# Kernel tuning notes

Measured on AMD Instinct MI355X. Metric: run time of the kernel, lower is better.

The kernel has to match this reference:

```python
import jax, jax.numpy as jnp
import numpy as np

N_NODES = 100000
N_EDGES = 1600000
D_IN = 64
HID = 64
N_GRAPHS = 256


def _glorot(key, shape):
    lim = float(np.sqrt(6.0 / (shape[0] + shape[1])))
    return jax.random.uniform(key, shape, jnp.float32, -lim, lim)


def setup_inputs() -> dict:
    key = jax.random.key(0)
    ks = jax.random.split(key, 12)
    x = jax.random.normal(ks[0], (N_NODES, D_IN), jnp.float32)
    edge_index = jax.random.randint(ks[1], (2, N_EDGES), 0, N_NODES, jnp.int64)
    batch = jnp.sort(jax.random.randint(ks[2], (N_NODES,), 0, N_GRAPHS, jnp.int64))
    params = {
        'Wrel1': _glorot(ks[3], (D_IN, HID)), 'brel1': jnp.zeros((HID,), jnp.float32), 'Wroot1': _glorot(ks[4], (D_IN, HID)),
        'Wrel2': _glorot(ks[5], (HID, HID)), 'brel2': jnp.zeros((HID,), jnp.float32), 'Wroot2': _glorot(ks[6], (HID, HID)),
        'Wrel3': _glorot(ks[7], (HID, HID)), 'brel3': jnp.zeros((HID,), jnp.float32), 'Wroot3': _glorot(ks[8], (HID, HID)),
        'Wlin': _glorot(ks[9], (HID, HID)), 'blin': jnp.zeros((HID,), jnp.float32),
    }
    return {'x': x, 'edge_index': edge_index, 'batch': batch, **params}


def _graph_conv(x, src, dst, Wrel, brel, Wroot):
    # PyG GraphConv: lin_rel(sum_{j in N(i)} x_j) + lin_root(x_i); bias on lin_rel only.
    aggr = jax.ops.segment_sum(x[src], dst, num_segments=N_NODES)  # [N, d] gather+scatter-add
    return aggr @ Wrel + brel + x @ Wroot


def reference(x, edge_index, batch, Wrel1, brel1, Wroot1, Wrel2, brel2, Wroot2,
              Wrel3, brel3, Wroot3, Wlin, blin):
    src, dst = edge_index[0], edge_index[1]
    h = jax.nn.relu(_graph_conv(x, src, dst, Wrel1, brel1, Wroot1))
    h = jax.nn.relu(_graph_conv(h, src, dst, Wrel2, brel2, Wroot2))
    h = _graph_conv(h, src, dst, Wrel3, brel3, Wroot3)
    # global_mean_pool over graphs
    sums = jax.ops.segment_sum(h, batch, num_segments=N_GRAPHS)          # [G, HID]
    counts = jax.ops.segment_sum(jnp.ones((N_NODES,), h.dtype), batch, num_segments=N_GRAPHS)
    pooled = sums / jnp.maximum(counts, 1.0)[:, None]
    # dropout is identity in eval mode
    return pooled @ Wlin + blin
```

## Files before the change

### kernel.cpp

```cpp
#include <hip/hip_runtime.h>
#include <hip/hip_bf16.h>

#define NN 100000
#define NE 1600000
#define DD 64
#define NG 256
#define SHIFT 8
#define NBK 391
#define BCAP 4608
#define NSB 256
#define CHUNK 6250

typedef __attribute__((ext_vector_type(8))) short bf16x8;
typedef __attribute__((ext_vector_type(4))) float f32x4;
typedef __attribute__((ext_vector_type(8))) unsigned short ushort8v;

__device__ __forceinline__ float b2f(ushort u){
  unsigned v = ((unsigned)u) << 16;
  return __uint_as_float(v);
}
__device__ __forceinline__ ushort f2b(float f){
  __hip_bfloat16 b = __float2bfloat16(f);
  return *(ushort*)&b;
}

__global__ void k_wpack3(const float* __restrict__ Wr1, const float* __restrict__ Wo1,
                         const float* __restrict__ Wr2, const float* __restrict__ Wo2,
                         const float* __restrict__ Wr3, const float* __restrict__ Wo3,
                         ushort* __restrict__ wp, int* __restrict__ gcur){
  int i = blockIdx.x*256 + threadIdx.x;
  if (i < NBK) gcur[i] = i*BCAP;
  if (i >= 3*8192) return;
  int lay = i >> 13;
  int r = i & 8191;
  int j = r & 7, l = (r>>3) & 63, t = (r>>9) & 7, s = r >> 12;
  int k = s*32 + ((l>>4)<<3) + j;
  int col = t*16 + (l&15);
  const float* Wrel  = (lay==0) ? Wr1 : (lay==1) ? Wr2 : Wr3;
  const float* Wroot = (lay==0) ? Wo1 : (lay==1) ? Wo2 : Wo3;
  float v = (col < 64) ? Wrel[k*64 + col] : Wroot[k*64 + (col-64)];
  wp[i] = f2b(v);
}

__global__ __launch_bounds__(512) void k_bscatter(const int* __restrict__ src, const int* __restrict__ dst,
                           int* __restrict__ gcur, unsigned* __restrict__ ebuf){
  __shared__ int h[NBK];
  __shared__ int base[NBK];
  __shared__ int lcur[NBK];
  for (int i=threadIdx.x; i<NBK; i+=512) h[i]=0;
  __syncthreads();
  const int e0 = blockIdx.x*CHUNK;
  const int e1 = min(e0+CHUNK, NE);
  for (int e=e0+threadIdx.x; e<e1; e+=512) atomicAdd(&h[dst[e]>>SHIFT], 1);
  __syncthreads();
  for (int i=threadIdx.x; i<NBK; i+=512){
    base[i] = h[i] ? atomicAdd(&gcur[i], h[i]) : 0;
    lcur[i] = 0;
  }
  __syncthreads();
  for (int e=e0+threadIdx.x; e<e1; e+=512){
    int d = dst[e];
    int b = d >> SHIFT;
    int r = atomicAdd(&lcur[b], 1);
    size_t idx = (size_t)base[b] + r;
    if (idx < (size_t)NBK*BCAP)
      ebuf[idx] = ((unsigned)(d & 255) << 17) | (unsigned)src[e];
  }
}

__global__ __launch_bounds__(512) void k_bfill(const unsigned* __restrict__ ebuf, const int* __restrict__ gcur,
                        int* __restrict__ rowptr, int* __restrict__ degarr, int* __restrict__ csr){
  __shared__ int c[256];
  __shared__ int lcur[256];
  __shared__ int s[256];
  __shared__ int scnt;
  const int b = blockIdx.x, t = threadIdx.x;
  const int ebase = b*BCAP;
  if (t == 0) scnt = min(gcur[b] - ebase, BCAP);
  if (t < 256) c[t] = 0;
  __syncthreads();
  const int cnt = scnt;
  for (int i=t; i<cnt; i+=512) atomicAdd(&c[ebuf[ebase+i]>>17], 1);
  __syncthreads();
  int v = (t < 256) ? c[t] : 0;
  if (t < 256) s[t] = v;
  __syncthreads();
  for (int off=1; off<256; off<<=1){
    int u = (t >= off && t < 256) ? s[t-off] : 0;
    __syncthreads();
    if (t < 256) s[t] += u;
    __syncthreads();
  }
  if (t < 256){
    int excl = s[t] - v;
    lcur[t] = excl;
    int node = (b << SHIFT) + t;
    if (node < NN){ rowptr[node] = ebase + excl; degarr[node] = v; }
  }
  __syncthreads();
  for (int i=t; i<cnt; i+=512){
    unsigned p = ebuf[ebase+i];
    int dl = (int)(p >> 17);
    int r = atomicAdd(&lcur[dl], 1);
    csr[ebase + r] = (int)(p & 0x1FFFFu);
  }
}

#define CPAD 136
__global__ __launch_bounds__(256) void k_gemm_mfma(const void* __restrict__ Av, int aIsF32,
    const ushort* __restrict__ wp, ushort* __restrict__ Y, ushort* __restrict__ Rr){
  __shared__ ushort ct[64*CPAD];
  const int tid = threadIdx.x;
  const int w = tid >> 6, l = tid & 63;
  const int m = l & 15, kg = l >> 4;
  const int row0 = blockIdx.x*64;
  int arow = row0 + w*16 + m; if (arow >= NN) arow = NN-1;
  bf16x8 a0, a1;
  if (aIsF32){
    const float* Af = (const float*)Av;
    float4 f0 = *(const float4*)&Af[(size_t)arow*64 + kg*8];
    float4 f1 = *(const float4*)&Af[(size_t)arow*64 + kg*8 + 4];
    float4 f2 = *(const float4*)&Af[(size_t)arow*64 + 32 + kg*8];
    float4 f3 = *(const float4*)&Af[(size_t)arow*64 + 32 + kg*8 + 4];
    a0[0]=(short)f2b(f0.x); a0[1]=(short)f2b(f0.y); a0[2]=(short)f2b(f0.z); a0[3]=(short)f2b(f0.w);
    a0[4]=(short)f2b(f1.x); a0[5]=(short)f2b(f1.y); a0[6]=(short)f2b(f1.z); a0[7]=(short)f2b(f1.w);
    a1[0]=(short)f2b(f2.x); a1[1]=(short)f2b(f2.y); a1[2]=(short)f2b(f2.z); a1[3]=(short)f2b(f2.w);
    a1[4]=(short)f2b(f3.x); a1[5]=(short)f2b(f3.y); a1[6]=(short)f2b(f3.z); a1[7]=(short)f2b(f3.w);
  } else {
    const ushort* Ab = (const ushort*)Av;
    a0 = *(const bf16x8*)&Ab[(size_t)arow*64 + kg*8];
    a1 = *(const bf16x8*)&Ab[(size_t)arow*64 + 32 + kg*8];
  }
  #pragma unroll
  for (int t=0; t<8; t++){
    bf16x8 b0 = *(const bf16x8*)&wp[((size_t)(0*8+t)*64 + l)*8];
    bf16x8 b1 = *(const bf16x8*)&wp[((size_t)(1*8+t)*64 + l)*8];
    f32x4 c = {0.f, 0.f, 0.f, 0.f};
    c = __builtin_amdgcn_mfma_f32_16x16x32_bf16(a0, b0, c, 0, 0, 0);
    c = __builtin_amdgcn_mfma_f32_16x16x32_bf16(a1, b1, c, 0, 0, 0);
    #pragma unroll
    for (int reg=0; reg<4; reg++){
      int lrow = w*16 + kg*4 + reg;
      ct[lrow*CPAD + t*16 + m] = f2b(c[reg]);
    }
  }
  __syncthreads();
  #pragma unroll
  for (int u=0; u<4; u++){
    int i = tid + u*256;
    int lrow = i >> 4, cb = i & 15;
    int grow = row0 + lrow;
    if (grow < NN){
      ushort8v v = *(const ushort8v*)&ct[lrow*CPAD + cb*8];
      if (cb < 8) *(ushort8v*)&Y [(size_t)grow*64 + cb*8]       = v;
      else        *(ushort8v*)&Rr[(size_t)grow*64 + (cb-8)*8]   = v;
    }
  }
}

__global__ __launch_bounds__(256) void k_aggr(const ushort* __restrict__ Y,
    const ushort* __restrict__ R, const float* __restrict__ brel,
    const int* __restrict__ rowptr, const int* __restrict__ degarr, const int* __restrict__ csr,
    ushort* __restrict__ hout, int do_relu){
  int node = blockIdx.x*4 + (threadIdx.x>>6);
  if (node >= NN) return;
  int lane = threadIdx.x & 63;
  int g = lane >> 3;
  int c8 = (lane & 7) << 3;
  int beg = rowptr[node];
  int dc = degarr[node];
  const int* lst = csr + beg;
  float a[8] = {0.f,0.f,0.f,0.f,0.f,0.f,0.f,0.f};
  int i = g;
  for (; i + 8 < dc; i += 16){
    int s0 = lst[i], s1 = lst[i+8];
    ushort8v y0 = *(const ushort8v*)&Y[((size_t)s0<<6) + c8];
    ushort8v y1 = *(const ushort8v*)&Y[((size_t)s1<<6) + c8];
    #pragma unroll
    for (int j=0;j<8;j++) a[j] += b2f(y0[j]) + b2f(y1[j]);
  }
  if (i < dc){
    int s0 = lst[i];
    ushort8v y0 = *(const ushort8v*)&Y[((size_t)s0<<6) + c8];
    #pragma unroll
    for (int j=0;j<8;j++) a[j] += b2f(y0[j]);
  }
  #pragma unroll
  for (int j=0;j<8;j++){
    a[j] += __shfl_xor(a[j], 8);
    a[j] += __shfl_xor(a[j], 16);
    a[j] += __shfl_xor(a[j], 32);
  }
  if (g == 0){
    ushort8v r8 = *(const ushort8v*)&R[((size_t)node<<6) + c8];
    float4 b0 = *(const float4*)&brel[c8];
    float4 b1 = *(const float4*)&brel[c8+4];
    float bb[8] = {b0.x,b0.y,b0.z,b0.w,b1.x,b1.y,b1.z,b1.w};
    ushort8v o;
    #pragma unroll
    for (int j=0;j<8;j++){
      float v = a[j] + b2f(r8[j]) + bb[j];
      if (do_relu) v = fmaxf(v, 0.f);
      o[j] = f2b(v);
    }
    *(ushort8v*)&hout[((size_t)node<<6) + c8] = o;
  }
}

__global__ __launch_bounds__(256) void k_pool(const ushort* __restrict__ h, const int* __restrict__ batch,
                       const float* __restrict__ Wlin, const float* __restrict__ blin,
                       float* __restrict__ out){
  int g = blockIdx.x;
  int lo=0, hi=NN;
  while (lo<hi){ int mid=(lo+hi)>>1; if (batch[mid] < g) lo=mid+1; else hi=mid; }
  int beg = lo;
  lo=0; hi=NN;
  while (lo<hi){ int mid=(lo+hi)>>1; if (batch[mid] < g+1) lo=mid+1; else hi=mid; }
  int end = lo;
  int lane = threadIdx.x & 63;
  int w = threadIdx.x >> 6;
  float acc = 0.f;
  for (int n = beg + w; n < end; n += 4) acc += b2f(h[(size_t)n*64 + lane]);
  __shared__ float red[4][64];
  __shared__ float p[64];
  red[w][lane] = acc;
  __syncthreads();
  if (w == 0){
    float v = red[0][lane]+red[1][lane]+red[2][lane]+red[3][lane];
    int cnt = end - beg;
    p[lane] = v / fmaxf((float)cnt, 1.f);
  }
  __syncthreads();
  if (w == 0){
    float o = blin[lane];
    #pragma unroll 8
    for (int k=0;k<64;k++) o += p[k]*Wlin[k*64+lane];
    out[g*64+lane] = o;
  }
}

extern "C" void kernel_launch(void* const* d_in, const int* in_sizes, int n_in,
                              void* d_out, int out_size, void* d_ws, size_t ws_size,
                              hipStream_t stream){
  const float* x     = (const float*)d_in[0];
  const int*   ei    = (const int*)  d_in[1];
  const int*   batch = (const int*)  d_in[2];
  const float* Wrel1 = (const float*)d_in[3];
  const float* brel1 = (const float*)d_in[4];
  const float* Wroot1= (const float*)d_in[5];
  const float* Wrel2 = (const float*)d_in[6];
  const float* brel2 = (const float*)d_in[7];
  const float* Wroot2= (const float*)d_in[8];
  const float* Wrel3 = (const float*)d_in[9];
  const float* brel3 = (const float*)d_in[10];
  const float* Wroot3= (const float*)d_in[11];
  const float* Wlin  = (const float*)d_in[12];
  const float* blin  = (const float*)d_in[13];
  const int* src = ei;
  const int* dst = ei + NE;

  char* wsB = (char*)d_ws;
  size_t off = 0;
  auto alloc = [&](size_t bytes)->void*{
    void* p = wsB + off; off = (off + bytes + 255) & ~(size_t)255; return p;
  };
  int*      csr    = (int*)     alloc((size_t)NBK*BCAP*4);
  unsigned* ebuf   = (unsigned*)alloc((size_t)NBK*BCAP*4);
  int*      rowptr = (int*)     alloc((size_t)NN*4);
  int*      degarr = (int*)     alloc((size_t)NN*4);
  int*      gcur   = (int*)     alloc(NBK*4);
  ushort*   wp     = (ushort*)  alloc((size_t)3*8192*2);
  ushort*   Y      = (ushort*)  alloc((size_t)NN*64*2);
  ushort*   R      = (ushort*)  alloc((size_t)NN*64*2);
  ushort*   h1     = (ushort*)  alloc((size_t)NN*64*2);
  ushort*   h2     = (ushort*)  alloc((size_t)NN*64*2);

  k_wpack3  <<<(3*8192+255)/256,256,0,stream>>>(Wrel1,Wroot1,Wrel2,Wroot2,Wrel3,Wroot3, wp, gcur);
  k_bscatter<<<NSB,512,0,stream>>>(src, dst, gcur, ebuf);
  k_bfill   <<<NBK,512,0,stream>>>(ebuf, gcur, rowptr, degarr, csr);

  int gb = (NN+63)/64;
  int ab = (NN+3)/4;

  k_gemm_mfma<<<gb,256,0,stream>>>(x,  1, wp + 0*8192, Y, R);
  k_aggr     <<<ab,256,0,stream>>>(Y, R, brel1, rowptr, degarr, csr, h1, 1);
  k_gemm_mfma<<<gb,256,0,stream>>>(h1, 0, wp + 1*8192, Y, R);
  k_aggr     <<<ab,256,0,stream>>>(Y, R, brel2, rowptr, degarr, csr, h2, 1);
  k_gemm_mfma<<<gb,256,0,stream>>>(h2, 0, wp + 2*8192, Y, R);
  k_aggr     <<<ab,256,0,stream>>>(Y, R, brel3, rowptr, degarr, csr, h1, 0);

  k_pool <<<NG,256,0,stream>>>(h1, batch, Wlin, blin, (float*)d_out);
}
```

Baseline: 241.7 us.

## Fuse CSR build stages with weight packing and first-layer GEMM into shared launches

Merges weight packing into the bucket-scatter kernel as extra blocks, and merges the bucket-fill CSR kernel with the first-layer MFMA GEMM in one launch. Block index picks the role, and a union shares LDS between the two roles. The bucket cursor is now zeroed with a memset and offset per bucket, removing one kernel and its initialisation work. The aim is fewer kernel launches and letting independent work run side by side. The cost is larger per-block LDS and 512-thread blocks for the GEMM tile, which may lower occupancy.

Measured after the change: 237.4 us. Within noise of the previous version (-1.8%).

```diff
diff --git a/kernel.cpp b/kernel.cpp
--- a/kernel.cpp
+++ b/kernel.cpp
@@ -10,6 +10,7 @@
 #define BCAP 4608
 #define NSB 256
 #define CHUNK 6250
+#define G1T 782
 
 typedef __attribute__((ext_vector_type(8))) short bf16x8;
 typedef __attribute__((ext_vector_type(4))) float f32x4;
@@ -24,26 +25,27 @@
   return *(ushort*)&b;
 }
 
-__global__ void k_wpack3(const float* __restrict__ Wr1, const float* __restrict__ Wo1,
+__global__ __launch_bounds__(512) void k_build1(const int* __restrict__ src, const int* __restrict__ dst,
+                         int* __restrict__ gcur, unsigned* __restrict__ ebuf,
+                         const float* __restrict__ Wr1, const float* __restrict__ Wo1,
                          const float* __restrict__ Wr2, const float* __restrict__ Wo2,
                          const float* __restrict__ Wr3, const float* __restrict__ Wo3,
-                         ushort* __restrict__ wp, int* __restrict__ gcur){
-  int i = blockIdx.x*256 + threadIdx.x;
-  if (i < NBK) gcur[i] = i*BCAP;
-  if (i >= 3*8192) return;
-  int lay = i >> 13;
-  int r = i & 8191;
-  int j = r & 7, l = (r>>3) & 63, t = (r>>9) & 7, s = r >> 12;
-  int k = s*32 + ((l>>4)<<3) + j;
-  int col = t*16 + (l&15);
-  const float* Wrel  = (lay==0) ? Wr1 : (lay==1) ? Wr2 : Wr3;
-  const float* Wroot = (lay==0) ? Wo1 : (lay==1) ? Wo2 : Wo3;
-  float v = (col < 64) ? Wrel[k*64 + col] : Wroot[k*64 + (col-64)];
-  wp[i] = f2b(v);
-}
-
-__global__ __launch_bounds__(512) void k_bscatter(const int* __restrict__ src, const int* __restrict__ dst,
-                           int* __restrict__ gcur, unsigned* __restrict__ ebuf){
+                         ushort* __restrict__ wp){
+  if (blockIdx.x >= NSB){
+    int i = (blockIdx.x - NSB)*512 + threadIdx.x;
+    if (i < 3*8192){
+      int lay = i >> 13;
+      int r = i & 8191;
+      int j = r & 7, l = (r>>3) & 63, t = (r>>9) & 7, s = r >> 12;
+      int k = s*32 + ((l>>4)<<3) + j;
+      int col = t*16 + (l&15);
+      const float* Wrel  = (lay==0) ? Wr1 : (lay==1) ? Wr2 : Wr3;
+      const float* Wroot = (lay==0) ? Wo1 : (lay==1) ? Wo2 : Wo3;
+      float v = (col < 64) ? Wrel[k*64 + col] : Wroot[k*64 + (col-64)];
+      wp[i] = f2b(v);
+    }
+    return;
+  }
   __shared__ int h[NBK];
   __shared__ int base[NBK];
   __shared__ int lcur[NBK];
@@ -54,7 +56,7 @@
   for (int e=e0+threadIdx.x; e<e1; e+=512) atomicAdd(&h[dst[e]>>SHIFT], 1);
   __syncthreads();
   for (int i=threadIdx.x; i<NBK; i+=512){
-    base[i] = h[i] ? atomicAdd(&gcur[i], h[i]) : 0;
+    base[i] = h[i] ? (i*BCAP + atomicAdd(&gcur[i], h[i])) : 0;
     lcur[i] = 0;
   }
   __syncthreads();
@@ -68,56 +70,59 @@
   }
 }
 
-__global__ __launch_bounds__(512) void k_bfill(const unsigned* __restrict__ ebuf, const int* __restrict__ gcur,
-                        int* __restrict__ rowptr, int* __restrict__ degarr, int* __restrict__ csr){
-  __shared__ int c[256];
-  __shared__ int lcur[256];
-  __shared__ int s[256];
-  __shared__ int scnt;
-  const int b = blockIdx.x, t = threadIdx.x;
-  const int ebase = b*BCAP;
-  if (t == 0) scnt = min(gcur[b] - ebase, BCAP);
-  if (t < 256) c[t] = 0;
-  __syncthreads();
-  const int cnt = scnt;
-  for (int i=t; i<cnt; i+=512) atomicAdd(&c[ebuf[ebase+i]>>17], 1);
-  __syncthreads();
-  int v = (t < 256) ? c[t] : 0;
-  if (t < 256) s[t] = v;
-  __syncthreads();
-  for (int off=1; off<256; off<<=1){
-    int u = (t >= off && t < 256) ? s[t-off] : 0;
+#define CPAD 136
+union BG {
+  struct { int c[256]; int lcur[256]; int s[256]; int scnt; } bf;
+  ushort ct[128*CPAD];
+};
+__global__ __launch_bounds__(512) void k_build2_gemm1(
+    const unsigned* __restrict__ ebuf, const int* __restrict__ gcur,
+    int* __restrict__ rowptr, int* __restrict__ degarr, int* __restrict__ csr,
+    const float* __restrict__ Af, const ushort* __restrict__ wp,
+    ushort* __restrict__ Y, ushort* __restrict__ Rr){
+  __shared__ BG sm;
+  const int t = threadIdx.x;
+  if (blockIdx.x < NBK){
+    const int b = blockIdx.x;
+    const int ebase = b*BCAP;
+    if (t == 0) sm.bf.scnt = min(gcur[b], BCAP);
+    if (t < 256) sm.bf.c[t] = 0;
     __syncthreads();
-    if (t < 256) s[t] += u;
+    const int cnt = sm.bf.scnt;
+    for (int i=t; i<cnt; i+=512) atomicAdd(&sm.bf.c[ebuf[ebase+i]>>17], 1);
     __syncthreads();
-  }
-  if (t < 256){
-    int excl = s[t] - v;
-    lcur[t] = excl;
-    int node = (b << SHIFT) + t;
-    if (node < NN){ rowptr[node] = ebase + excl; degarr[node] = v; }
-  }
-  __syncthreads();
-  for (int i=t; i<cnt; i+=512){
-    unsigned p = ebuf[ebase+i];
-    int dl = (int)(p >> 17);
-    int r = atomicAdd(&lcur[dl], 1);
-    csr[ebase + r] = (int)(p & 0x1FFFFu);
-  }
-}
-
-#define CPAD 136
-__global__ __launch_bounds__(256) void k_gemm_mfma(const void* __restrict__ Av, int aIsF32,
-    const ushort* __restrict__ wp, ushort* __restrict__ Y, ushort* __restrict__ Rr){
-  __shared__ ushort ct[64*CPAD];
-  const int tid = threadIdx.x;
-  const int w = tid >> 6, l = tid & 63;
+    int v = (t < 256) ? sm.bf.c[t] : 0;
+    if (t < 256) sm.bf.s[t] = v;
+    __syncthreads();
+    for (int off=1; off<256; off<<=1){
+      int u = (t >= off && t < 256) ? sm.bf.s[t-off] : 0;
+      __syncthreads();
+      if (t < 256) sm.bf.s[t] += u;
+      __syncthreads();
+    }
+    if (t < 256){
+      int excl = sm.bf.s[t] - v;
+      sm.bf.lcur[t] = excl;
+      int node = (b << SHIFT) + t;
+      if (node < NN){ rowptr[node] = ebase + excl; degarr[node] = v; }
+    }
+    __syncthreads();
+    for (int i=t; i<cnt; i+=512){
+      unsigned p = ebuf[ebase+i];
+      int dl = (int)(p >> 17);
+      int r = atomicAdd(&sm.bf.lcur[dl], 1);
+      csr[ebase + r] = (int)(p & 0x1FFFFu);
+    }
+    return;
+  }
+  const int tile = blockIdx.x - NBK;
+  if (tile >= G1T) return;
+  const int w = t >> 6, l = t & 63;
   const int m = l & 15, kg = l >> 4;
-  const int row0 = blockIdx.x*64;
+  const int row0 = tile*128;
   int arow = row0 + w*16 + m; if (arow >= NN) arow = NN-1;
   bf16x8 a0, a1;
-  if (aIsF32){
-    const float* Af = (const float*)Av;
+  {
     float4 f0 = *(const float4*)&Af[(size_t)arow*64 + kg*8];
     float4 f1 = *(const float4*)&Af[(size_t)arow*64 + kg*8 + 4];
     float4 f2 = *(const float4*)&Af[(size_t)arow*64 + 32 + kg*8];
@@ -126,11 +131,44 @@
     a0[4]=(short)f2b(f1.x); a0[5]=(short)f2b(f1.y); a0[6]=(short)f2b(f1.z); a0[7]=(short)f2b(f1.w);
     a1[0]=(short)f2b(f2.x); a1[1]=(short)f2b(f2.y); a1[2]=(short)f2b(f2.z); a1[3]=(short)f2b(f2.w);
     a1[4]=(short)f2b(f3.x); a1[5]=(short)f2b(f3.y); a1[6]=(short)f2b(f3.z); a1[7]=(short)f2b(f3.w);
-  } else {
-    const ushort* Ab = (const ushort*)Av;
-    a0 = *(const bf16x8*)&Ab[(size_t)arow*64 + kg*8];
-    a1 = *(const bf16x8*)&Ab[(size_t)arow*64 + 32 + kg*8];
-  }
+  }
+  #pragma unroll
+  for (int tt=0; tt<8; tt++){
+    bf16x8 b0 = *(const bf16x8*)&wp[((size_t)(0*8+tt)*64 + l)*8];
+    bf16x8 b1 = *(const bf16x8*)&wp[((size_t)(1*8+tt)*64 + l)*8];
+    f32x4 c = {0.f, 0.f, 0.f, 0.f};
+    c = __builtin_amdgcn_mfma_f32_16x16x32_bf16(a0, b0, c, 0, 0, 0);
+    c = __builtin_amdgcn_mfma_f32_16x16x32_bf16(a1, b1, c, 0, 0, 0);
+    #pragma unroll
+    for (int reg=0; reg<4; reg++){
+      int lrow = w*16 + kg*4 + reg;
+      sm.ct[lrow*CPAD + tt*16 + m] = f2b(c[reg]);
+    }
+  }
+  __syncthreads();
+  #pragma unroll
+  for (int u=0; u<4; u++){
+    int i = t + u*512;
+    int lrow = i >> 4, cb = i & 15;
+    int grow = row0 + lrow;
+    if (grow < NN){
+      ushort8v v = *(const ushort8v*)&sm.ct[lrow*CPAD + cb*8];
+      if (cb < 8) *(ushort8v*)&Y [(size_t)grow*64 + cb*8]       = v;
+      else        *(ushort8v*)&Rr[(size_t)grow*64 + (cb-8)*8]   = v;
+    }
+  }
+}
+
+__global__ __launch_bounds__(256) void k_gemm_mfma(const ushort* __restrict__ Ab,
+    const ushort* __restrict__ wp, ushort* __restrict__ Y, ushort* __restrict__ Rr){
+  __shared__ ushort ct[64*CPAD];
+  const int tid = threadIdx.x;
+  const int w = tid >> 6, l = tid & 63;
+  const int m = l & 15, kg = l >> 4;
+  const int row0 = blockIdx.x*64;
+  int arow = row0 + w*16 + m; if (arow >= NN) arow = NN-1;
+  bf16x8 a0 = *(const bf16x8*)&Ab[(size_t)arow*64 + kg*8];
+  bf16x8 a1 = *(const bf16x8*)&Ab[(size_t)arow*64 + 32 + kg*8];
   #pragma unroll
   for (int t=0; t<8; t++){
     bf16x8 b0 = *(const bf16x8*)&wp[((size_t)(0*8+t)*64 + l)*8];
@@ -275,18 +313,19 @@
   ushort*   h1     = (ushort*)  alloc((size_t)NN*64*2);
   ushort*   h2     = (ushort*)  alloc((size_t)NN*64*2);
 
-  k_wpack3  <<<(3*8192+255)/256,256,0,stream>>>(Wrel1,Wroot1,Wrel2,Wroot2,Wrel3,Wroot3, wp, gcur);
-  k_bscatter<<<NSB,512,0,stream>>>(src, dst, gcur, ebuf);
-  k_bfill   <<<NBK,512,0,stream>>>(ebuf, gcur, rowptr, degarr, csr);
+  hipMemsetAsync(gcur, 0, NBK*4, stream);
+  k_build1<<<NSB + 49, 512, 0, stream>>>(src, dst, gcur, ebuf,
+                                         Wrel1,Wroot1,Wrel2,Wroot2,Wrel3,Wroot3, wp);
+  k_build2_gemm1<<<NBK + G1T, 512, 0, stream>>>(ebuf, gcur, rowptr, degarr, csr,
+                                                x, wp + 0*8192, Y, R);
 
   int gb = (NN+63)/64;
   int ab = (NN+3)/4;
 
-  k_gemm_mfma<<<gb,256,0,stream>>>(x,  1, wp + 0*8192, Y, R);
   k_aggr     <<<ab,256,0,stream>>>(Y, R, brel1, rowptr, degarr, csr, h1, 1);
-  k_gemm_mfma<<<gb,256,0,stream>>>(h1, 0, wp + 1*8192, Y, R);
+  k_gemm_mfma<<<gb,256,0,stream>>>(h1, wp + 1*8192, Y, R);
   k_aggr     <<<ab,256,0,stream>>>(Y, R, brel2, rowptr, degarr, csr, h2, 1);
-  k_gemm_mfma<<<gb,256,0,stream>>>(h2, 0, wp + 2*8192, Y, R);
+  k_gemm_mfma<<<gb,256,0,stream>>>(h2, wp + 2*8192, Y, R);
   k_aggr     <<<ab,256,0,stream>>>(Y, R, brel3, rowptr, degarr, csr, h1, 0);
 
   k_pool <<<NG,256,0,stream>>>(h1, batch, Wlin, blin, (float*)d_out);
```
